# Kernel optimization log

Hardware: AMD Instinct MI355X
Metric: run time of the kernel (lower is better)

The kernel has to match this reference:

```python
import jax, jax.numpy as jnp
import numpy as np

B, L, D, H, E = 64, 128, 768, 2, 131072  # graphs, nodes/graph, hidden, heads, edges
N = B * L
C = D // H  # per-head channels


def _transformer_conv(x, src, dst, wq, bq, wk, bk, wv, bv, ws, bs):
    # PyG TransformerConv (concat=True, root_weight=True, beta=False)
    n = x.shape[0]
    q = (x @ wq + bq).reshape(n, H, C)
    k = (x @ wk + bk).reshape(n, H, C)
    v = (x @ wv + bv).reshape(n, H, C)
    # per-edge attention logits [E, H]
    logits = jnp.sum(q[dst] * k[src], axis=-1) * (1.0 / np.sqrt(C))
    # scatter softmax over incoming edges of each dst node
    m = jax.ops.segment_max(logits, dst, num_segments=n)
    e = jnp.exp(logits - m[dst])
    s = jax.ops.segment_sum(e, dst, num_segments=n)
    alpha = e / s[dst]  # [E, H]
    msg = alpha[..., None] * v[src]  # [E, H, C]
    agg = jax.ops.segment_sum(msg, dst, num_segments=n).reshape(n, D)
    return agg + x @ ws + bs


def setup_inputs() -> dict:
    key = jax.random.key(0)
    ks = jax.random.split(key, 24)
    x = jax.random.normal(ks[0], (N, D), jnp.float32)
    # within-graph random edges
    dst = jax.random.randint(ks[1], (E,), 0, N)
    off = jax.random.randint(ks[2], (E,), 0, L)
    src = (dst // L) * L + off
    edge_index = jnp.stack([src, dst]).astype(jnp.int32)

    def lin(k, i, o):
        return jax.random.normal(k, (i, o), jnp.float32) * 0.02

    inp = {"x": x, "edge_index": edge_index}
    i = 3
    for layer in ("1", "2"):
        for nm in ("wq", "wk", "wv", "ws"):
            inp[nm + layer] = lin(ks[i], D, D); i += 1
            inp["b" + nm[1] + layer] = jnp.zeros((D,), jnp.float32)
    inp["atti_w"] = lin(ks[i], 2 * D, D); i += 1
    inp["atti_b"] = jnp.zeros((D,), jnp.float32)
    inp["atts_w"] = lin(ks[i], D, 1); i += 1
    inp["atts_b"] = jnp.zeros((1,), jnp.float32)
    inp["fc1_w"] = lin(ks[i], D, D); i += 1
    inp["fc1_b"] = jnp.zeros((D,), jnp.float32)
    inp["fc2_w"] = lin(ks[i], D, 3); i += 1
    inp["fc2_b"] = jnp.zeros((3,), jnp.float32)
    return inp


def reference(x, edge_index, wq1, bq1, wk1, bk1, wv1, bv1, ws1, bs1,
              wq2, bq2, wk2, bk2, wv2, bv2, ws2, bs2,
              atti_w, atti_b, atts_w, atts_b, fc1_w, fc1_b, fc2_w, fc2_b):
    src, dst = edge_index[0], edge_index[1]
    h = jax.nn.relu(_transformer_conv(x, src, dst, wq1, bq1, wk1, bk1, wv1, bv1, ws1, bs1))
    h = jax.nn.relu(_transformer_conv(h, src, dst, wq2, bq2, wk2, bk2, wv2, bv2, ws2, bs2))
    # pad(): equal-size graphs -> reshape, mask all-valid (x_mask all False)
    hp = h.reshape(B, L, D)
    # attention pooling (eval path): query = first node of each graph
    x_q = jnp.broadcast_to(hp[:, :1], hp.shape)  # [B, L, D]
    x_c = jax.nn.relu(jnp.concatenate([x_q, hp], axis=-1) @ atti_w + atti_b)
    score = x_c @ atts_w + atts_b  # [B, L, 1]
    score = jax.nn.softmax(score, axis=1)
    pooled = jnp.sum(hp * score, axis=1)  # [B, D]
    out = jnp.tanh(pooled @ fc1_w + fc1_b) @ fc2_w + fc2_b
    return jax.nn.log_softmax(out, axis=-1)
```

## Files before the change

kernel.cpp:

```cpp
#include <hip/hip_runtime.h>

#define NN 8192
#define DD 768
#define EE 131072
#define BBg 64
#define LLn 128
#define CCh 384

typedef unsigned short u16;
typedef unsigned char u8;
typedef __attribute__((ext_vector_type(8))) short short8;
typedef __attribute__((ext_vector_type(4))) float f32x4;

__device__ __forceinline__ float b2f(u16 u) {
    union { unsigned int i; float f; } x; x.i = ((unsigned int)u) << 16; return x.f;
}
__device__ __forceinline__ u16 f2b(float f) {
    union { float f; unsigned int i; } x; x.f = f;
    unsigned int r = x.i + 0x7fffu + ((x.i >> 16) & 1u);
    return (u16)(r >> 16);
}
__device__ __forceinline__ void gload16(const void* g, void* l) {
    __builtin_amdgcn_global_load_lds((const __attribute__((address_space(1))) void*)g,
                                     (__attribute__((address_space(3))) void*)l, 16, 0, 0);
}

__global__ __launch_bounds__(256) void prep_kernel(const float* __restrict__ in,
                                                   u16* __restrict__ out,
                                                   unsigned int* __restrict__ cnt32,
                                                   float* __restrict__ score) {
    int i = blockIdx.x * 256 + threadIdx.x;
    float4 v = ((const float4*)in)[i];
    ushort4 o; o.x = f2b(v.x); o.y = f2b(v.y); o.z = f2b(v.z); o.w = f2b(v.w);
    ((ushort4*)out)[i] = o;
    if (blockIdx.x < 1024) cnt32[i] = 0;
    else if (blockIdx.x < 1056) score[i - 1024 * 256] = 0.f;
}

struct TP { const float* src; u16* dst; int rowOff; };
struct TP11 { TP a[11]; };

__global__ __launch_bounds__(256) void combo_kernel(TP11 args,
                                                    const int* __restrict__ srcp,
                                                    const int* __restrict__ dstp,
                                                    unsigned int* __restrict__ cnt32) {
    __shared__ float tile[64][65];
    if (blockIdx.z == 11) {
        for (int e = blockIdx.x * 256 + threadIdx.x; e < EE; e += 144 * 256) {
            int d = dstp[e], s = srcp[e];
            int g = d >> 7;
            int idx = (g << 14) + ((d & 127) << 7) + (s & 127);
            atomicAdd(&cnt32[idx >> 2], 1u << ((idx & 3) * 8));
        }
        return;
    }
    TP tp = args.a[blockIdx.z];
    int bx = blockIdx.x % 12, by = blockIdx.x / 12;
    int n0 = bx * 64, k0 = by * 64;
    int t = threadIdx.x;
    int tc = t & 63, tr = t >> 6;
#pragma unroll
    for (int i = 0; i < 16; i++)
        tile[tr + i * 4][tc] = tp.src[(size_t)(tp.rowOff + k0 + tr + i * 4) * DD + n0 + tc];
    __syncthreads();
#pragma unroll
    for (int i = 0; i < 16; i++) {
        int row = tr + i * 4;
        tp.dst[(size_t)(n0 + row) * DD + k0 + tc] = f2b(tile[tc][row]);
    }
}

enum { EPI_F32 = 1, EPI_TANH = 3 };

__global__ __launch_bounds__(256) void gemm_bf16(const u16* __restrict__ A,
                                                 const u16* __restrict__ Wt,
                                                 const float* __restrict__ bias,
                                                 void* __restrict__ outp, int K, int mode) {
    __shared__ u16 As[64][72];
    __shared__ u16 Bs[64][72];
    const int m0 = blockIdx.y * 64, n0 = blockIdx.x * 64;
    const int t = threadIdx.x;
    const int lane = t & 63, w = t >> 6;
    const int tr = t >> 2, tc = (t & 3) * 16;
    f32x4 acc[4] = {{0,0,0,0},{0,0,0,0},{0,0,0,0},{0,0,0,0}};
    const int fRow = lane & 15;
    const int fK = (lane >> 4) * 8;

    for (int k0 = 0; k0 < K; k0 += 64) {
        int4 a0 = *(const int4*)(A + (size_t)(m0 + tr) * K + k0 + tc);
        int4 a1 = *(const int4*)(A + (size_t)(m0 + tr) * K + k0 + tc + 8);
        int4 b0 = *(const int4*)(Wt + (size_t)(n0 + tr) * K + k0 + tc);
        int4 b1 = *(const int4*)(Wt + (size_t)(n0 + tr) * K + k0 + tc + 8);
        __syncthreads();
        *(int4*)&As[tr][tc] = a0; *(int4*)&As[tr][tc + 8] = a1;
        *(int4*)&Bs[tr][tc] = b0; *(int4*)&Bs[tr][tc + 8] = b1;
        __syncthreads();
#pragma unroll
        for (int s = 0; s < 2; s++) {
            short8 af = *(const short8*)&As[w * 16 + fRow][s * 32 + fK];
#pragma unroll
            for (int g = 0; g < 4; g++) {
                short8 bf = *(const short8*)&Bs[g * 16 + fRow][s * 32 + fK];
                acc[g] = __builtin_amdgcn_mfma_f32_16x16x32_bf16(af, bf, acc[g], 0, 0, 0);
            }
        }
    }
    const int colLocal = lane & 15;
    const int rowLocal = (lane >> 4) * 4;
#pragma unroll
    for (int g = 0; g < 4; g++) {
        int col = n0 + g * 16 + colLocal;
        float bv = bias ? bias[col] : 0.f;
#pragma unroll
        for (int i = 0; i < 4; i++) {
            int row = m0 + w * 16 + rowLocal + i;
            float v = acc[g][i] + bv;
            if (mode == EPI_TANH) v = tanhf(v);
            ((float*)outp)[(size_t)row * DD + col] = v;
        }
    }
}

#define SLAB 24576
__global__ __launch_bounds__(512, 2) void gemm256(const u16* __restrict__ A,
                                                  const u16* __restrict__ Wt,
                                                  const float* __restrict__ b0,
                                                  const float* __restrict__ b1,
                                                  const float* __restrict__ b2,
                                                  const float* __restrict__ b3,
                                                  u16* __restrict__ o0, u16* __restrict__ o1,
                                                  u16* __restrict__ o2, u16* __restrict__ o3) {
    __shared__ u16 smem[3 * SLAB];
    const int K = DD;
    const int t = threadIdx.x;
    const int lane = t & 63, w = t >> 6;
    const int wr = w >> 1, wc = w & 1;
    const int id = blockIdx.y * 24 + blockIdx.x;
    const int xcd = id & 7, jj = id >> 3;
    const int by = (xcd >> 1) * 8 + jj / 12;
    const int bx = (xcd & 1) * 12 + jj % 12;
    const int m0 = by * 256, n0 = bx * 128;
    const int fRow = lane & 15, fThr = lane >> 4;
    const u16* Abase = A + (size_t)m0 * K;
    const u16* Bbase = Wt + (size_t)n0 * K;

    auto stage = [&](u16* slab, int kt2) {
        const int k0 = kt2 * 64;
#pragma unroll
        for (int s = 0; s < 4; ++s) {
            int c = t + 512 * s;
            int row = c >> 3;
            int col = ((c & 7) ^ (row & 7)) * 8;
            gload16(Abase + (size_t)row * K + k0 + col, (char*)slab + (size_t)c * 16);
        }
#pragma unroll
        for (int s = 0; s < 2; ++s) {
            int c = t + 512 * s;
            int row = c >> 3;
            int col = ((c & 7) ^ (row & 7)) * 8;
            gload16(Bbase + (size_t)row * K + k0 + col, (char*)(slab + 16384) + (size_t)c * 16);
        }
    };
    auto loadFrags = [&](const u16* As, const u16* Bs, int p, short8* af, short8* bf) {
        const int cj = p * 4 + fThr;
#pragma unroll
        for (int i = 0; i < 4; ++i) {
            const int R = wr * 64 + i * 16 + fRow;
            af[i] = *(const short8*)&As[((size_t)R * 8 + (cj ^ (R & 7))) * 8];
        }
#pragma unroll
        for (int g = 0; g < 4; ++g) {
            const int Rb = wc * 64 + g * 16 + fRow;
            bf[g] = *(const short8*)&Bs[((size_t)Rb * 8 + (cj ^ (Rb & 7))) * 8];
        }
    };

    stage(smem, 0);
    stage(smem + SLAB, 1);
    asm volatile("s_waitcnt vmcnt(6)" ::: "memory");
    __builtin_amdgcn_s_barrier();

    short8 afA[4], bfA[4], afB[4], bfB[4];
    loadFrags(smem, smem + 16384, 0, afA, bfA);

    f32x4 acc[4][4] = {};
    int cur = 0;
    for (int kt = 0; kt < 12; ++kt) {
        const u16* As = smem + cur * SLAB;
        const u16* Bs = As + 16384;
        int nx = cur + 2; if (nx >= 3) nx -= 3;
        int pv = cur + 1; if (pv >= 3) pv -= 3;
        if (kt < 10) stage(smem + nx * SLAB, kt + 2);

        loadFrags(As, Bs, 1, afB, bfB);
        asm volatile("s_waitcnt lgkmcnt(8)" ::: "memory");
        __builtin_amdgcn_sched_barrier(0);
        __builtin_amdgcn_s_setprio(1);
#pragma unroll
        for (int i = 0; i < 4; ++i)
#pragma unroll
            for (int g = 0; g < 4; ++g)
                acc[i][g] = __builtin_amdgcn_mfma_f32_16x16x32_bf16(afA[i], bfA[g], acc[i][g], 0, 0, 0);
        __builtin_amdgcn_s_setprio(0);

        if (kt < 10) asm volatile("s_waitcnt vmcnt(6)" ::: "memory");
        else         asm volatile("s_waitcnt vmcnt(0)" ::: "memory");
        __builtin_amdgcn_s_barrier();

        if (kt < 11) {
            loadFrags(smem + pv * SLAB, smem + pv * SLAB + 16384, 0, afA, bfA);
            asm volatile("s_waitcnt lgkmcnt(8)" ::: "memory");
        } else {
            asm volatile("s_waitcnt lgkmcnt(0)" ::: "memory");
        }
        __builtin_amdgcn_sched_barrier(0);
        __builtin_amdgcn_s_setprio(1);
#pragma unroll
        for (int i = 0; i < 4; ++i)
#pragma unroll
            for (int g = 0; g < 4; ++g)
                acc[i][g] = __builtin_amdgcn_mfma_f32_16x16x32_bf16(afB[i], bfB[g], acc[i][g], 0, 0, 0);
        __builtin_amdgcn_s_setprio(0);
        __builtin_amdgcn_s_barrier();

        cur = pv;
    }

    const int chunk = n0 / DD;
    const float* bp = (chunk == 0) ? b0 : (chunk == 1) ? b1 : (chunk == 2) ? b2 : b3;
    u16* op = (chunk == 0) ? o0 : (chunk == 1) ? o1 : (chunk == 2) ? o2 : o3;
    const int cb0 = n0 - chunk * DD;
    if (chunk == 2) {
        u16 (*Vt)[264] = (u16(*)[264])smem;
#pragma unroll
        for (int g = 0; g < 4; g++) {
            float bv = bp[cb0 + wc * 64 + g * 16 + fRow];
#pragma unroll
            for (int i = 0; i < 4; i++)
#pragma unroll
                for (int rr = 0; rr < 4; rr++)
                    Vt[wc * 64 + g * 16 + fRow][wr * 64 + i * 16 + fThr * 4 + rr] =
                        f2b(acc[i][g][rr] + bv);
        }
        __syncthreads();
#pragma unroll
        for (int ii = 0; ii < 16; ii++) {
            int c = t + 512 * ii;
            int col = c >> 6, ch = c & 63;
            *(ushort4*)(op + (size_t)(cb0 + col) * NN + m0 + ch * 4) =
                *(const ushort4*)&Vt[col][ch * 4];
        }
    } else {
        u16 (*Cs)[136] = (u16(*)[136])smem;
#pragma unroll
        for (int g = 0; g < 4; g++) {
            float bv = bp[cb0 + wc * 64 + g * 16 + fRow];
#pragma unroll
            for (int i = 0; i < 4; i++)
#pragma unroll
                for (int rr = 0; rr < 4; rr++)
                    Cs[wr * 64 + i * 16 + fThr * 4 + rr][wc * 64 + g * 16 + fRow] =
                        f2b(acc[i][g][rr] + bv);
        }
        __syncthreads();
#pragma unroll
        for (int ii = 0; ii < 16; ii++) {
            int c = t + 512 * ii;
            int row = c >> 5, ch = c & 31;
            *(ushort4*)(op + (size_t)(m0 + row) * DD + cb0 + ch * 4) =
                *(const ushort4*)&Cs[row][ch * 4];
        }
    }
}

__global__ __launch_bounds__(256) void gemm_xc(const u16* __restrict__ A,
                                               const u16* __restrict__ Wt,
                                               const u16* __restrict__ wt8,
                                               const float* __restrict__ atti_b,
                                               const float* __restrict__ atts_w,
                                               float* __restrict__ score) {
    __shared__ u16 As[128 * 64];
    __shared__ u16 Bs[128 * 64];
    __shared__ float aq_p[2][128];
    const int K = DD;
    const int t = threadIdx.x;
    const int lane = t & 63, w = t >> 6;
    const int wr = w >> 1, wc = w & 1;
    const int n0 = blockIdx.x * 128, m0 = blockIdx.y * 128;
    const int fRow = lane & 15, fThr = lane >> 4;

    {
        int col = t & 127, kh = t >> 7;
        const u16* xr = A + (size_t)m0 * DD + kh * 384;
        const u16* wr8 = wt8 + (size_t)(n0 + col) * DD + kh * 384;
        float s = 0.f;
#pragma unroll 8
        for (int j = 0; j < 96; j++) {
            ushort4 a4 = *(const ushort4*)(xr + j * 4);
            ushort4 b4 = *(const ushort4*)(wr8 + j * 4);
            s += b2f(a4.x) * b2f(b4.x) + b2f(a4.y) * b2f(b4.y)
               + b2f(a4.z) * b2f(b4.z) + b2f(a4.w) * b2f(b4.w);
        }
        aq_p[kh][col] = s;
    }

    f32x4 acc[4][4] = {};
    const u16* Abase = A + (size_t)m0 * K;
    const u16* Bbase = Wt + (size_t)n0 * K;
    for (int k0 = 0; k0 < K; k0 += 64) {
        __syncthreads();
#pragma unroll
        for (int i = 0; i < 4; i++) {
            int c = t + 256 * i;
            int row = c >> 3;
            int col = ((c & 7) ^ (row & 7)) * 8;
            gload16(Abase + (size_t)row * K + k0 + col, (char*)As + (size_t)c * 16);
            gload16(Bbase + (size_t)row * K + k0 + col, (char*)Bs + (size_t)c * 16);
        }
        __syncthreads();
#pragma unroll
        for (int kk = 0; kk < 64; kk += 32) {
            const int cjW = (kk >> 3) + fThr;
            short8 af[4], bf[4];
#pragma unroll
            for (int i = 0; i < 4; i++) {
                int R = wr * 64 + i * 16 + fRow;
                af[i] = *(const short8*)&As[(R * 8 + (cjW ^ (R & 7))) * 8];
            }
#pragma unroll
            for (int g = 0; g < 4; g++) {
                int R = wc * 64 + g * 16 + fRow;
                bf[g] = *(const short8*)&Bs[(R * 8 + (cjW ^ (R & 7))) * 8];
            }
#pragma unroll
            for (int i = 0; i < 4; i++)
#pragma unroll
                for (int g = 0; g < 4; g++)
                    acc[i][g] = __builtin_amdgcn_mfma_f32_16x16x32_bf16(af[i], bf[g], acc[i][g], 0, 0, 0);
        }
    }
    float rsum[4][4] = {};
#pragma unroll
    for (int g = 0; g < 4; g++) {
        int cl = wc * 64 + g * 16 + fRow;
        int col = n0 + cl;
        float bv = atti_b[col] + aq_p[0][cl] + aq_p[1][cl];
        float av = atts_w[col];
#pragma unroll
        for (int i = 0; i < 4; i++)
#pragma unroll
            for (int rr = 0; rr < 4; rr++) {
                float v = fmaxf(acc[i][g][rr] + bv, 0.f);
                rsum[i][rr] += v * av;
            }
    }
#pragma unroll
    for (int i = 0; i < 4; i++)
#pragma unroll
        for (int rr = 0; rr < 4; rr++) {
            float s = rsum[i][rr];
            s += __shfl_xor(s, 1, 16); s += __shfl_xor(s, 2, 16);
            s += __shfl_xor(s, 4, 16); s += __shfl_xor(s, 8, 16);
            if (fRow == 0)
                atomicAdd(&score[m0 + wr * 64 + i * 16 + fThr * 4 + rr], s);
        }
}

__global__ __launch_bounds__(256, 2) void attn_fused(const u16* __restrict__ qb,
                                                  const u16* __restrict__ kb,
                                                  const u16* __restrict__ vT,
                                                  const u8* __restrict__ cnt,
                                                  const u16* __restrict__ hs,
                                                  u16* __restrict__ out) {
    __shared__ u16 As[64][72];
    __shared__ u16 Bs[128][72];
    __shared__ u16 Pl[64][136];
    __shared__ u16 Vt[64][136];
    const int half = blockIdx.x, hd = blockIdx.y;
    const int g = blockIdx.z >> 1, ch = blockIdx.z & 1;
    const int t = threadIdx.x;
    const int lane = t & 63, w = t >> 6;
    const int fRow = lane & 15, fThr = lane >> 4;
    const int dstBase = g * 128 + half * 64;
    const u16* Qb = qb + (size_t)dstBase * DD + hd * CCh;
    const u16* Kb = kb + (size_t)(g * 128) * DD + hd * CCh;

    f32x4 acc[8] = {};
    const int trA = t >> 2, tcA = (t & 3) * 16;
    const int trB = t >> 1, tcB = (t & 1) * 32;
    for (int k0 = 0; k0 < CCh; k0 += 64) {
        int4 a0 = *(const int4*)(Qb + (size_t)trA * DD + k0 + tcA);
        int4 a1 = *(const int4*)(Qb + (size_t)trA * DD + k0 + tcA + 8);
        int4 b0 = *(const int4*)(Kb + (size_t)trB * DD + k0 + tcB);
        int4 b1 = *(const int4*)(Kb + (size_t)trB * DD + k0 + tcB + 8);
        int4 b2 = *(const int4*)(Kb + (size_t)trB * DD + k0 + tcB + 16);
        int4 b3 = *(const int4*)(Kb + (size_t)trB * DD + k0 + tcB + 24);
        __syncthreads();
        *(int4*)&As[trA][tcA] = a0; *(int4*)&As[trA][tcA + 8] = a1;
        *(int4*)&Bs[trB][tcB] = b0; *(int4*)&Bs[trB][tcB + 8] = b1;
        *(int4*)&Bs[trB][tcB + 16] = b2; *(int4*)&Bs[trB][tcB + 24] = b3;
        __syncthreads();
#pragma unroll
        for (int kk = 0; kk < 64; kk += 32) {
            short8 af = *(const short8*)&As[w * 16 + fRow][kk + fThr * 8];
#pragma unroll
            for (int j = 0; j < 8; j++) {
                short8 bf = *(const short8*)&Bs[j * 16 + fRow][kk + fThr * 8];
                acc[j] = __builtin_amdgcn_mfma_f32_16x16x32_bf16(af, bf, acc[j], 0, 0, 0);
            }
        }
    }

    const float scale = 0.05103103630798288f;
    const u8* cg = cnt + ((size_t)g << 14);
    const int rbase = half * 64 + w * 16 + fThr * 4;
    float pv[8][4];
#pragma unroll
    for (int i = 0; i < 4; i++) {
        float m = -3.4e38f;
#pragma unroll
        for (int j = 0; j < 8; j++) {
            float c = (float)cg[(rbase + i) * 128 + j * 16 + fRow];
            float s = acc[j][i] * scale;
            pv[j][i] = c;
            if (c > 0.f) m = fmaxf(m, s);
        }
#pragma unroll
        for (int msk = 1; msk <= 8; msk <<= 1) m = fmaxf(m, __shfl_xor(m, msk, 16));
        float sum = 0.f;
#pragma unroll
        for (int j = 0; j < 8; j++) {
            float p = (pv[j][i] > 0.f) ? pv[j][i] * __expf(acc[j][i] * scale - m) : 0.f;
            pv[j][i] = p; sum += p;
        }
#pragma unroll
        for (int msk = 1; msk <= 8; msk <<= 1) sum += __shfl_xor(sum, msk, 16);
        float inv = (sum > 0.f) ? 1.f / sum : 0.f;
#pragma unroll
        for (int j = 0; j < 8; j++)
            Pl[w * 16 + fThr * 4 + i][j * 16 + fRow] = f2b(pv[j][i] * inv);
    }

    for (int cc = ch * 3; cc < ch * 3 + 3; cc++) {
        __syncthreads();
#pragma unroll
        for (int ii = 0; ii < 4; ii++) {
            int q = t + 256 * ii;
            int row = q >> 4, col = (q & 15) * 8;
            *(int4*)&Vt[row][col] =
                *(const int4*)(vT + (size_t)(hd * CCh + cc * 64 + row) * NN + g * 128 + col);
        }
        __syncthreads();
        f32x4 acc2[4] = {};
#pragma unroll
        for (int kk = 0; kk < 128; kk += 32) {
            short8 af = *(const short8*)&Pl[w * 16 + fRow][kk + fThr * 8];
#pragma unroll
            for (int j = 0; j < 4; j++) {
                short8 bf = *(const short8*)&Vt[j * 16 + fRow][kk + fThr * 8];
                acc2[j] = __builtin_amdgcn_mfma_f32_16x16x32_bf16(af, bf, acc2[j], 0, 0, 0);
            }
        }
#pragma unroll
        for (int j = 0; j < 4; j++) {
            int c = hd * CCh + cc * 64 + j * 16 + fRow;
#pragma unroll
            for (int i = 0; i < 4; i++) {
                int row = dstBase + w * 16 + fThr * 4 + i;
                size_t idx = (size_t)row * DD + c;
                float r = fmaxf(acc2[j][i] + b2f(hs[idx]), 0.f);
                out[idx] = f2b(r);
            }
        }
    }
}

__global__ __launch_bounds__(192) void pool_kernel(const float* __restrict__ score,
                                                   const u16* __restrict__ hx,
                                                   u16* __restrict__ pb) {
    int b = blockIdx.x, t = threadIdx.x;
    __shared__ float sprob[LLn];
    if (t < 64) {
        float s0 = score[b * LLn + t];
        float s1 = score[b * LLn + 64 + t];
        float mx = fmaxf(s0, s1);
#pragma unroll
        for (int m = 1; m <= 32; m <<= 1) mx = fmaxf(mx, __shfl_xor(mx, m, 64));
        float e0 = __expf(s0 - mx), e1 = __expf(s1 - mx);
        float sum = e0 + e1;
#pragma unroll
        for (int m = 1; m <= 32; m <<= 1) sum += __shfl_xor(sum, m, 64);
        float inv = 1.f / sum;
        sprob[t] = e0 * inv; sprob[t + 64] = e1 * inv;
    }
    __syncthreads();
    int c = t * 4;
    float a0 = 0, a1 = 0, a2 = 0, a3 = 0;
    for (int l = 0; l < LLn; l++) {
        float wl = sprob[l];
        ushort4 hv = *(const ushort4*)(hx + (size_t)(b * LLn + l) * DD + c);
        a0 += wl * b2f(hv.x); a1 += wl * b2f(hv.y); a2 += wl * b2f(hv.z); a3 += wl * b2f(hv.w);
    }
    ushort4 o; o.x = f2b(a0); o.y = f2b(a1); o.z = f2b(a2); o.w = f2b(a3);
    *(ushort4*)(pb + (size_t)b * DD + c) = o;
}

__global__ __launch_bounds__(256) void head2_kernel(const float* __restrict__ u,
                                                    const float* __restrict__ fc2w,
                                                    const float* __restrict__ fc2b,
                                                    float* __restrict__ outp) {
    int b = blockIdx.x, t = threadIdx.x;
    __shared__ float sred[4][3];
    float p0 = 0, p1 = 0, p2 = 0;
    for (int k = t; k < DD; k += 256) {
        float uv = u[(size_t)b * DD + k];
        p0 += uv * fc2w[k * 3 + 0]; p1 += uv * fc2w[k * 3 + 1]; p2 += uv * fc2w[k * 3 + 2];
    }
#pragma unroll
    for (int m = 1; m <= 32; m <<= 1) {
        p0 += __shfl_xor(p0, m, 64); p1 += __shfl_xor(p1, m, 64); p2 += __shfl_xor(p2, m, 64);
    }
    int w = t >> 6, lane = t & 63;
    if (lane == 0) { sred[w][0] = p0; sred[w][1] = p1; sred[w][2] = p2; }
    __syncthreads();
    if (t == 0) {
        float z0 = fc2b[0], z1 = fc2b[1], z2 = fc2b[2];
        for (int i = 0; i < 4; i++) { z0 += sred[i][0]; z1 += sred[i][1]; z2 += sred[i][2]; }
        float mx = fmaxf(z0, fmaxf(z1, z2));
        float lse = mx + logf(__expf(z0 - mx) + __expf(z1 - mx) + __expf(z2 - mx));
        outp[b * 3 + 0] = z0 - lse; outp[b * 3 + 1] = z1 - lse; outp[b * 3 + 2] = z2 - lse;
    }
}

static inline char* carve(char*& p, size_t bytes) {
    char* r = p;
    p += (bytes + 255) & ~(size_t)255;
    return r;
}

extern "C" void kernel_launch(void* const* d_in, const int* in_sizes, int n_in,
                              void* d_out, int out_size, void* d_ws, size_t ws_size,
                              hipStream_t stream) {
    const float* x = (const float*)d_in[0];
    const int* ei = (const int*)d_in[1];
    const int* srcp = ei;
    const int* dstp = ei + EE;
    const float* wL[8] = {(const float*)d_in[2], (const float*)d_in[4], (const float*)d_in[6],
                          (const float*)d_in[8], (const float*)d_in[10], (const float*)d_in[12],
                          (const float*)d_in[14], (const float*)d_in[16]};
    const float* bL[8] = {(const float*)d_in[3], (const float*)d_in[5], (const float*)d_in[7],
                          (const float*)d_in[9], (const float*)d_in[11], (const float*)d_in[13],
                          (const float*)d_in[15], (const float*)d_in[17]};
    const float* atti_w = (const float*)d_in[18];
    const float* atti_b = (const float*)d_in[19];
    const float* atts_w = (const float*)d_in[20];
    const float* fc1_w = (const float*)d_in[22];
    const float* fc1_b = (const float*)d_in[23];
    const float* fc2_w = (const float*)d_in[24];
    const float* fc2_b = (const float*)d_in[25];
    float* outp = (float*)d_out;

    char* p = (char*)d_ws;
    const size_t ndb = (size_t)NN * DD * 2;
    const size_t wsz = (size_t)DD * DD * 2;
    u16* qb = (u16*)carve(p, ndb);
    u16* kb = (u16*)carve(p, ndb);
    u16* vt = (u16*)carve(p, ndb);
    u16* xb = (u16*)carve(p, ndb);
    u16* hb = (u16*)carve(p, ndb);
    u16* hs = (u16*)carve(p, ndb);
    u16* wtcat1 = (u16*)carve(p, wsz * 4);
    u16* wtcat2 = (u16*)carve(p, wsz * 4);
    u16* wt8 = (u16*)carve(p, wsz);
    u16* wt9 = (u16*)carve(p, wsz);
    u16* wtfc1 = (u16*)carve(p, wsz);
    u16* pb = (u16*)carve(p, (size_t)BBg * DD * 2);
    float* uu = (float*)carve(p, (size_t)BBg * DD * 4);
    u8* cnt = (u8*)carve(p, (size_t)BBg * 128 * 128);
    float* score = (float*)carve(p, NN * 4);

    prep_kernel<<<6144, 256, 0, stream>>>(x, xb, (unsigned int*)cnt, score);

    TP11 tps;
    for (int i = 0; i < 4; i++) tps.a[i] = {wL[i], wtcat1 + (size_t)i * DD * DD, 0};
    for (int i = 0; i < 4; i++) tps.a[4 + i] = {wL[4 + i], wtcat2 + (size_t)i * DD * DD, 0};
    tps.a[8] = {atti_w, wt8, 0};
    tps.a[9] = {atti_w, wt9, DD};
    tps.a[10] = {fc1_w, wtfc1, 0};
    combo_kernel<<<dim3(144, 1, 12), 256, 0, stream>>>(tps, srcp, dstp, (unsigned int*)cnt);

    dim3 gf(24, 32);
    dim3 ga(2, 2, BBg * 2);
    gemm256<<<gf, 512, 0, stream>>>(xb, wtcat1, bL[0], bL[1], bL[2], bL[3], qb, kb, vt, hs);
    attn_fused<<<ga, 256, 0, stream>>>(qb, kb, vt, cnt, hs, hb);
    gemm256<<<gf, 512, 0, stream>>>(hb, wtcat2, bL[4], bL[5], bL[6], bL[7], qb, kb, vt, hs);
    attn_fused<<<ga, 256, 0, stream>>>(qb, kb, vt, cnt, hs, xb);

    gemm_xc<<<dim3(6, 64), 256, 0, stream>>>(xb, wt9, wt8, atti_b, atts_w, score);

    pool_kernel<<<BBg, 192, 0, stream>>>(score, xb, pb);
    gemm_bf16<<<dim3(12, 1), 256, 0, stream>>>(pb, wtfc1, fc1_b, uu, DD, EPI_TANH);
    head2_kernel<<<BBg, 256, 0, stream>>>(uu, fc2_w, fc2_b, outp);
}
```

Before: 335.5 us.

## Load attention MFMA operands directly from global memory and widen pooling grid

The QK^T stage of the fused attention kernel now loads Q fragments into registers once and streams K fragments straight from global memory into MFMA operands, double-buffered across k-steps. This replaces the shared-memory staging and its barriers. The P·V stage reads V fragments directly from global memory instead of staging tiles in LDS. The pooling kernel is split across three channel chunks per graph to launch more blocks, at the cost of scalar loads and recomputing the softmax in every chunk. The aim is to remove LDS traffic and syncs, but it raises register pressure and relies on caches to absorb the redundant global reads.

```diff
diff --git a/kernel.cpp b/kernel.cpp
--- a/kernel.cpp
+++ b/kernel.cpp
@@ -367,15 +367,12 @@
 }
 
 __global__ __launch_bounds__(256, 2) void attn_fused(const u16* __restrict__ qb,
-                                                  const u16* __restrict__ kb,
-                                                  const u16* __restrict__ vT,
-                                                  const u8* __restrict__ cnt,
-                                                  const u16* __restrict__ hs,
-                                                  u16* __restrict__ out) {
-    __shared__ u16 As[64][72];
-    __shared__ u16 Bs[128][72];
+                                                     const u16* __restrict__ kb,
+                                                     const u16* __restrict__ vT,
+                                                     const u8* __restrict__ cnt,
+                                                     const u16* __restrict__ hs,
+                                                     u16* __restrict__ out) {
     __shared__ u16 Pl[64][136];
-    __shared__ u16 Vt[64][136];
     const int half = blockIdx.x, hd = blockIdx.y;
     const int g = blockIdx.z >> 1, ch = blockIdx.z & 1;
     const int t = threadIdx.x;
@@ -385,28 +382,40 @@
     const u16* Qb = qb + (size_t)dstBase * DD + hd * CCh;
     const u16* Kb = kb + (size_t)(g * 128) * DD + hd * CCh;
 
+    const u16* Qrow = Qb + (size_t)(w * 16 + fRow) * DD + fThr * 8;
+    short8 qf[12];
+#pragma unroll
+    for (int s = 0; s < 12; ++s) qf[s] = *(const short8*)(Qrow + s * 32);
+
+    const u16* Krow = Kb + fThr * 8;
+    short8 bp[8], bq[8];
+#pragma unroll
+    for (int j = 0; j < 8; ++j)
+        bp[j] = *(const short8*)(Krow + (size_t)(j * 16 + fRow) * DD);
+#pragma unroll
+    for (int j = 0; j < 8; ++j)
+        bq[j] = *(const short8*)(Krow + (size_t)(j * 16 + fRow) * DD + 32);
+
     f32x4 acc[8] = {};
-    const int trA = t >> 2, tcA = (t & 3) * 16;
-    const int trB = t >> 1, tcB = (t & 1) * 32;
-    for (int k0 = 0; k0 < CCh; k0 += 64) {
-        int4 a0 = *(const int4*)(Qb + (size_t)trA * DD + k0 + tcA);
-        int4 a1 = *(const int4*)(Qb + (size_t)trA * DD + k0 + tcA + 8);
-        int4 b0 = *(const int4*)(Kb + (size_t)trB * DD + k0 + tcB);
-        int4 b1 = *(const int4*)(Kb + (size_t)trB * DD + k0 + tcB + 8);
-        int4 b2 = *(const int4*)(Kb + (size_t)trB * DD + k0 + tcB + 16);
-        int4 b3 = *(const int4*)(Kb + (size_t)trB * DD + k0 + tcB + 24);
-        __syncthreads();
-        *(int4*)&As[trA][tcA] = a0; *(int4*)&As[trA][tcA + 8] = a1;
-        *(int4*)&Bs[trB][tcB] = b0; *(int4*)&Bs[trB][tcB + 8] = b1;
-        *(int4*)&Bs[trB][tcB + 16] = b2; *(int4*)&Bs[trB][tcB + 24] = b3;
-        __syncthreads();
-#pragma unroll
-        for (int kk = 0; kk < 64; kk += 32) {
-            short8 af = *(const short8*)&As[w * 16 + fRow][kk + fThr * 8];
-#pragma unroll
-            for (int j = 0; j < 8; j++) {
-                short8 bf = *(const short8*)&Bs[j * 16 + fRow][kk + fThr * 8];
-                acc[j] = __builtin_amdgcn_mfma_f32_16x16x32_bf16(af, bf, acc[j], 0, 0, 0);
+#pragma unroll
+    for (int s = 0; s < 12; ++s) {
+        if ((s & 1) == 0) {
+#pragma unroll
+            for (int j = 0; j < 8; ++j)
+                acc[j] = __builtin_amdgcn_mfma_f32_16x16x32_bf16(qf[s], bp[j], acc[j], 0, 0, 0);
+            if (s + 2 < 12) {
+#pragma unroll
+                for (int j = 0; j < 8; ++j)
+                    bp[j] = *(const short8*)(Krow + (size_t)(j * 16 + fRow) * DD + (s + 2) * 32);
+            }
+        } else {
+#pragma unroll
+            for (int j = 0; j < 8; ++j)
+                acc[j] = __builtin_amdgcn_mfma_f32_16x16x32_bf16(qf[s], bq[j], acc[j], 0, 0, 0);
+            if (s + 2 < 12) {
+#pragma unroll
+                for (int j = 0; j < 8; ++j)
+                    bq[j] = *(const short8*)(Krow + (size_t)(j * 16 + fRow) * DD + (s + 2) * 32);
             }
         }
     }
@@ -442,22 +451,14 @@
     }
 
     for (int cc = ch * 3; cc < ch * 3 + 3; cc++) {
-        __syncthreads();
-#pragma unroll
-        for (int ii = 0; ii < 4; ii++) {
-            int q = t + 256 * ii;
-            int row = q >> 4, col = (q & 15) * 8;
-            *(int4*)&Vt[row][col] =
-                *(const int4*)(vT + (size_t)(hd * CCh + cc * 64 + row) * NN + g * 128 + col);
-        }
-        __syncthreads();
+        const u16* Vb = vT + (size_t)(hd * CCh + cc * 64) * NN + g * 128 + fThr * 8;
         f32x4 acc2[4] = {};
 #pragma unroll
         for (int kk = 0; kk < 128; kk += 32) {
             short8 af = *(const short8*)&Pl[w * 16 + fRow][kk + fThr * 8];
 #pragma unroll
             for (int j = 0; j < 4; j++) {
-                short8 bf = *(const short8*)&Vt[j * 16 + fRow][kk + fThr * 8];
+                short8 bf = *(const short8*)(Vb + (size_t)(j * 16 + fRow) * NN + kk);
                 acc2[j] = __builtin_amdgcn_mfma_f32_16x16x32_bf16(af, bf, acc2[j], 0, 0, 0);
             }
         }
@@ -475,10 +476,10 @@
     }
 }
 
-__global__ __launch_bounds__(192) void pool_kernel(const float* __restrict__ score,
+__global__ __launch_bounds__(256) void pool_kernel(const float* __restrict__ score,
                                                    const u16* __restrict__ hx,
                                                    u16* __restrict__ pb) {
-    int b = blockIdx.x, t = threadIdx.x;
+    int chunk = blockIdx.x, b = blockIdx.y, t = threadIdx.x;
     __shared__ float sprob[LLn];
     if (t < 64) {
         float s0 = score[b * LLn + t];
@@ -494,15 +495,11 @@
         sprob[t] = e0 * inv; sprob[t + 64] = e1 * inv;
     }
     __syncthreads();
-    int c = t * 4;
-    float a0 = 0, a1 = 0, a2 = 0, a3 = 0;
-    for (int l = 0; l < LLn; l++) {
-        float wl = sprob[l];
-        ushort4 hv = *(const ushort4*)(hx + (size_t)(b * LLn + l) * DD + c);
-        a0 += wl * b2f(hv.x); a1 += wl * b2f(hv.y); a2 += wl * b2f(hv.z); a3 += wl * b2f(hv.w);
-    }
-    ushort4 o; o.x = f2b(a0); o.y = f2b(a1); o.z = f2b(a2); o.w = f2b(a3);
-    *(ushort4*)(pb + (size_t)b * DD + c) = o;
+    int c = chunk * 256 + t;
+    float a = 0.f;
+    for (int l = 0; l < LLn; l++)
+        a += sprob[l] * b2f(hx[(size_t)(b * LLn + l) * DD + c]);
+    pb[(size_t)b * DD + c] = f2b(a);
 }
 
 __global__ __launch_bounds__(256) void head2_kernel(const float* __restrict__ u,
@@ -598,7 +595,7 @@
 
     gemm_xc<<<dim3(6, 64), 256, 0, stream>>>(xb, wt9, wt8, atti_b, atts_w, score);
 
-    pool_kernel<<<BBg, 192, 0, stream>>>(score, xb, pb);
+    pool_kernel<<<dim3(3, BBg), 256, 0, stream>>>(score, xb, pb);
     gemm_bf16<<<dim3(12, 1), 256, 0, stream>>>(pb, wtfc1, fc1_b, uu, DD, EPI_TANH);
     head2_kernel<<<BBg, 256, 0, stream>>>(uu, fc2_w, fc2_b, outp);
 }
```

Result: slower. 367.4 us (+9.5%).

## Split-K the fc1 GEMM and widen pooling grid for more parallelism

Applied to the files above, without the earlier changes.

The fc1 GEMM used to run on only 12 blocks. It is now split into 6 K-slices (72 blocks), each writing partial sums, and head2 reduces them and adds the bias and tanh. The pooling kernel moves from 64 blocks to 192 (3 channel chunks per graph) with scalar loads per thread. Both changes target low occupancy in the tail kernels, at the cost of a larger partial-sum buffer and extra reads in head2.

```diff
diff --git a/kernel.cpp b/kernel.cpp
--- a/kernel.cpp
+++ b/kernel.cpp
@@ -70,15 +70,13 @@
     }
 }
 
-enum { EPI_F32 = 1, EPI_TANH = 3 };
-
-__global__ __launch_bounds__(256) void gemm_bf16(const u16* __restrict__ A,
-                                                 const u16* __restrict__ Wt,
-                                                 const float* __restrict__ bias,
-                                                 void* __restrict__ outp, int K, int mode) {
+__global__ __launch_bounds__(256) void fc1_kernel(const u16* __restrict__ A,
+                                                  const u16* __restrict__ Wt,
+                                                  float* __restrict__ uu) {
     __shared__ u16 As[64][72];
     __shared__ u16 Bs[64][72];
-    const int m0 = blockIdx.y * 64, n0 = blockIdx.x * 64;
+    const int n0 = blockIdx.x * 64;
+    const int kz = blockIdx.y;
     const int t = threadIdx.x;
     const int lane = t & 63, w = t >> 6;
     const int tr = t >> 2, tc = (t & 3) * 16;
@@ -86,11 +84,11 @@
     const int fRow = lane & 15;
     const int fK = (lane >> 4) * 8;
 
-    for (int k0 = 0; k0 < K; k0 += 64) {
-        int4 a0 = *(const int4*)(A + (size_t)(m0 + tr) * K + k0 + tc);
-        int4 a1 = *(const int4*)(A + (size_t)(m0 + tr) * K + k0 + tc + 8);
-        int4 b0 = *(const int4*)(Wt + (size_t)(n0 + tr) * K + k0 + tc);
-        int4 b1 = *(const int4*)(Wt + (size_t)(n0 + tr) * K + k0 + tc + 8);
+    for (int k0 = kz * 128; k0 < kz * 128 + 128; k0 += 64) {
+        int4 a0 = *(const int4*)(A + (size_t)tr * DD + k0 + tc);
+        int4 a1 = *(const int4*)(A + (size_t)tr * DD + k0 + tc + 8);
+        int4 b0 = *(const int4*)(Wt + (size_t)(n0 + tr) * DD + k0 + tc);
+        int4 b1 = *(const int4*)(Wt + (size_t)(n0 + tr) * DD + k0 + tc + 8);
         __syncthreads();
         *(int4*)&As[tr][tc] = a0; *(int4*)&As[tr][tc + 8] = a1;
         *(int4*)&Bs[tr][tc] = b0; *(int4*)&Bs[tr][tc + 8] = b1;
@@ -110,13 +108,10 @@
 #pragma unroll
     for (int g = 0; g < 4; g++) {
         int col = n0 + g * 16 + colLocal;
-        float bv = bias ? bias[col] : 0.f;
 #pragma unroll
         for (int i = 0; i < 4; i++) {
-            int row = m0 + w * 16 + rowLocal + i;
-            float v = acc[g][i] + bv;
-            if (mode == EPI_TANH) v = tanhf(v);
-            ((float*)outp)[(size_t)row * DD + col] = v;
+            int row = w * 16 + rowLocal + i;
+            uu[(size_t)kz * 64 * DD + (size_t)row * DD + col] = acc[g][i];
         }
     }
 }
@@ -475,10 +470,10 @@
     }
 }
 
-__global__ __launch_bounds__(192) void pool_kernel(const float* __restrict__ score,
+__global__ __launch_bounds__(256) void pool_kernel(const float* __restrict__ score,
                                                    const u16* __restrict__ hx,
                                                    u16* __restrict__ pb) {
-    int b = blockIdx.x, t = threadIdx.x;
+    int chunk = blockIdx.x, b = blockIdx.y, t = threadIdx.x;
     __shared__ float sprob[LLn];
     if (t < 64) {
         float s0 = score[b * LLn + t];
@@ -494,18 +489,15 @@
         sprob[t] = e0 * inv; sprob[t + 64] = e1 * inv;
     }
     __syncthreads();
-    int c = t * 4;
-    float a0 = 0, a1 = 0, a2 = 0, a3 = 0;
-    for (int l = 0; l < LLn; l++) {
-        float wl = sprob[l];
-        ushort4 hv = *(const ushort4*)(hx + (size_t)(b * LLn + l) * DD + c);
-        a0 += wl * b2f(hv.x); a1 += wl * b2f(hv.y); a2 += wl * b2f(hv.z); a3 += wl * b2f(hv.w);
-    }
-    ushort4 o; o.x = f2b(a0); o.y = f2b(a1); o.z = f2b(a2); o.w = f2b(a3);
-    *(ushort4*)(pb + (size_t)b * DD + c) = o;
+    int c = chunk * 256 + t;
+    float a = 0.f;
+    for (int l = 0; l < LLn; l++)
+        a += sprob[l] * b2f(hx[(size_t)(b * LLn + l) * DD + c]);
+    pb[(size_t)b * DD + c] = f2b(a);
 }
 
 __global__ __launch_bounds__(256) void head2_kernel(const float* __restrict__ u,
+                                                    const float* __restrict__ fc1b,
                                                     const float* __restrict__ fc2w,
                                                     const float* __restrict__ fc2b,
                                                     float* __restrict__ outp) {
@@ -513,7 +505,11 @@
     __shared__ float sred[4][3];
     float p0 = 0, p1 = 0, p2 = 0;
     for (int k = t; k < DD; k += 256) {
-        float uv = u[(size_t)b * DD + k];
+        float a = fc1b[k];
+#pragma unroll
+        for (int s = 0; s < 6; ++s)
+            a += u[(size_t)s * 64 * DD + (size_t)b * DD + k];
+        float uv = tanhf(a);
         p0 += uv * fc2w[k * 3 + 0]; p1 += uv * fc2w[k * 3 + 1]; p2 += uv * fc2w[k * 3 + 2];
     }
 #pragma unroll
@@ -575,7 +571,7 @@
     u16* wt9 = (u16*)carve(p, wsz);
     u16* wtfc1 = (u16*)carve(p, wsz);
     u16* pb = (u16*)carve(p, (size_t)BBg * DD * 2);
-    float* uu = (float*)carve(p, (size_t)BBg * DD * 4);
+    float* uu = (float*)carve(p, (size_t)BBg * DD * 4 * 6);
     u8* cnt = (u8*)carve(p, (size_t)BBg * 128 * 128);
     float* score = (float*)carve(p, NN * 4);
 
@@ -598,7 +594,7 @@
 
     gemm_xc<<<dim3(6, 64), 256, 0, stream>>>(xb, wt9, wt8, atti_b, atts_w, score);
 
-    pool_kernel<<<BBg, 192, 0, stream>>>(score, xb, pb);
-    gemm_bf16<<<dim3(12, 1), 256, 0, stream>>>(pb, wtfc1, fc1_b, uu, DD, EPI_TANH);
-    head2_kernel<<<BBg, 256, 0, stream>>>(uu, fc2_w, fc2_b, outp);
-}
+    pool_kernel<<<dim3(3, BBg), 256, 0, stream>>>(score, xb, pb);
+    fc1_kernel<<<dim3(12, 6), 256, 0, stream>>>(pb, wtfc1, uu);
+    head2_kernel<<<BBg, 256, 0, stream>>>(uu, fc1_b, fc2_w, fc2_b, outp);
+}
```

Result: faster. 327.4 us (-2.4%).
